# Optimization experiments

Measured on AMD Instinct MI355X. Metric: run time of the kernel, lower is better.

## Reference

```python
import jax, jax.numpy as jnp
import numpy as np

B, N, D, H, DEPTH, MLP_DIM = 8, 1024, 256, 8, 4, 1024
INNER = D * H  # quirk of this repo: inner_dim = dim * n_heads
LN_EPS = 1e-3  # keras LayerNormalization default epsilon


def setup_inputs() -> dict:
    key = jax.random.key(0)
    ks = jax.random.split(key, 6)
    def nrm(k, shape, s=0.02):
        return jax.random.normal(k, shape, dtype=jnp.float32) * s
    return {
        "x": jax.random.normal(ks[0], (B, N, D), dtype=jnp.float32),
        # PreNorm LayerNorm(axis=1): params have shape (N,) per layer
        "ln1_g": jnp.ones((DEPTH, N), jnp.float32),
        "ln1_b": jnp.zeros((DEPTH, N), jnp.float32),
        "w_qkv": nrm(ks[1], (DEPTH, D, 3 * INNER)),
        "w_out": nrm(ks[2], (DEPTH, INNER, D)),
        "b_out": jnp.zeros((DEPTH, D), jnp.float32),
        "ln2_g": jnp.ones((DEPTH, N), jnp.float32),
        "ln2_b": jnp.zeros((DEPTH, N), jnp.float32),
        "w1": nrm(ks[3], (DEPTH, D, MLP_DIM)),
        "b1": jnp.zeros((DEPTH, MLP_DIM), jnp.float32),
        "w2": nrm(ks[4], (DEPTH, MLP_DIM, D)),
        "b2": jnp.zeros((DEPTH, D), jnp.float32),
    }


def _ln_axis1(x, g, b):
    # keras LayerNormalization(axis=1): normalize over sequence axis
    mu = jnp.mean(x, axis=1, keepdims=True)
    var = jnp.var(x, axis=1, keepdims=True)
    return (x - mu) * jax.lax.rsqrt(var + LN_EPS) * g[None, :, None] + b[None, :, None]


def _split_heads(t):
    # b n (h d) -> b h n d, with per-head dim d == D
    return t.reshape(B, N, H, D).transpose(0, 2, 1, 3)


def reference(x, ln1_g, ln1_b, w_qkv, w_out, b_out, ln2_g, ln2_b, w1, b1, w2, b2):
    scale = D ** -0.5
    for i in range(DEPTH):
        # --- PreNorm + MHA ---
        h = _ln_axis1(x, ln1_g[i], ln1_b[i])
        qkv = h @ w_qkv[i]                               # [B,N,3*INNER]
        q, k, v = jnp.split(qkv, 3, axis=-1)
        q, k, v = _split_heads(q), _split_heads(k), _split_heads(v)
        dot = jnp.einsum('bhid,bhjd->bhij', q, k) * scale  # [B,H,N,N]
        A = jax.nn.softmax(dot, axis=-1)
        z = jnp.einsum('bhij,bhjd->bhid', A, v)
        z = z.transpose(0, 2, 1, 3).reshape(B, N, INNER)
        x = x + z @ w_out[i] + b_out[i]
        # --- PreNorm + MLP (exact erf GELU) ---
        h = _ln_axis1(x, ln2_g[i], ln2_b[i])
        h = jax.nn.gelu(h @ w1[i] + b1[i], approximate=False)
        x = x + h @ w2[i] + b2[i]
    return x
```

## Files before the change

kernel.cpp:

```cpp
#include <hip/hip_runtime.h>
#include <hip/hip_bf16.h>

#define SEQ    1024
#define DM     256
#define NH     8
#define NB     8
#define NLAYER 4
#define MLPD   1024
#define ROWS   (NB*SEQ)
#define QKVW   6144
#define INNERW 2048

typedef __attribute__((ext_vector_type(8))) short bh8;
typedef __attribute__((ext_vector_type(4))) short bh4;
typedef __attribute__((ext_vector_type(4))) float fx4;

__device__ __forceinline__ short f2bf(float f) {
  return __builtin_bit_cast(short, __float2bfloat16(f));
}
__device__ __forceinline__ fx4 mfma16(bh8 a, bh8 b, fx4 c) {
  return __builtin_amdgcn_mfma_f32_16x16x32_bf16(a, b, c, 0, 0, 0);
}
__device__ __forceinline__ void g2l16(const void* g, void* l) {
  __builtin_amdgcn_global_load_lds(
      (const __attribute__((address_space(1))) void*)g,
      (__attribute__((address_space(3))) void*)l, 16, 0, 0);
}
__device__ __forceinline__ int kperm(int r) {
  return ((r & 1) << 2) | ((r >> 1) & 3);
}

__global__ void wtrans_k(const float* __restrict__ src, __hip_bfloat16* __restrict__ dst,
                         int R, int C, size_t sls, size_t dls) {
  src += (size_t)blockIdx.z * sls;
  dst += (size_t)blockIdx.z * dls;
  __shared__ float t[32][33];
  int tx = threadIdx.x, ty = threadIdx.y;
  int r0 = blockIdx.y * 32, c0 = blockIdx.x * 32;
#pragma unroll
  for (int i = 0; i < 32; i += 8) t[ty + i][tx] = src[(size_t)(r0 + ty + i) * C + c0 + tx];
  __syncthreads();
#pragma unroll
  for (int i = 0; i < 32; i += 8)
    dst[(size_t)(c0 + ty + i) * R + r0 + tx] = __float2bfloat16(t[tx][ty + i]);
}

__global__ void ln_k(const float* __restrict__ xf, const float* __restrict__ gam,
                     const float* __restrict__ bet, __hip_bfloat16* __restrict__ h) {
  int b = blockIdx.y, d0 = blockIdx.x * 8;
  int dl = threadIdx.x & 1;
  int nt = threadIdx.x >> 1;
  const float* xb = xf + (size_t)b * SEQ * DM + d0 + dl * 4;
  fx4 s = 0.f, ss = 0.f;
  for (int n = nt; n < SEQ; n += 128) {
    fx4 v = *(const fx4*)(xb + (size_t)n * DM);
    s += v; ss += v * v;
  }
  __shared__ fx4 S1[128][2], S2[128][2];
  __shared__ fx4 MU[2], RS[2];
  S1[nt][dl] = s; S2[nt][dl] = ss;
  __syncthreads();
  if (nt < 16) {
    fx4 a = S1[nt][dl], c = S2[nt][dl];
#pragma unroll
    for (int i = 0; i < 7; i++) { a += S1[nt + 16 + i * 16][dl]; c += S2[nt + 16 + i * 16][dl]; }
    S1[nt][dl] = a; S2[nt][dl] = c;
  }
  __syncthreads();
  if (nt == 0) {
    fx4 a = 0.f, c = 0.f;
#pragma unroll
    for (int i = 0; i < 16; i++) { a += S1[i][dl]; c += S2[i][dl]; }
    fx4 mu, rs;
#pragma unroll
    for (int r = 0; r < 4; r++) {
      mu[r] = a[r] * (1.f / SEQ);
      float var = c[r] * (1.f / SEQ) - mu[r] * mu[r];
      rs[r] = rsqrtf(var + 1e-3f);
    }
    MU[dl] = mu; RS[dl] = rs;
  }
  __syncthreads();
  fx4 mu = MU[dl], rs = RS[dl];
  __hip_bfloat16* hb = h + (size_t)b * SEQ * DM + d0 + dl * 4;
  for (int n = nt; n < SEQ; n += 128) {
    fx4 v = *(const fx4*)(xb + (size_t)n * DM);
    float gn = gam[n], bn = bet[n];
    bh4 o;
#pragma unroll
    for (int r = 0; r < 4; r++) o[r] = f2bf((v[r] - mu[r]) * rs[r] * gn + bn);
    *(bh4*)(hb + (size_t)n * DM) = o;
  }
}

template <int BM, int BN, int EPI, int DBUF>
__global__ __launch_bounds__(256) void gemm_bt(
    const __hip_bfloat16* __restrict__ A, const __hip_bfloat16* __restrict__ Bt,
    __hip_bfloat16* __restrict__ Cout, const float* __restrict__ bias,
    const float* __restrict__ rin, float* __restrict__ rout,
    __hip_bfloat16* __restrict__ vT, int M, int Nc, int K) {
  constexpr int BK = 64;
  constexpr int NR = BN / 32;
  constexpr int MR = BM / 32;
  constexpr int SPAN = (BM + BN) * BK;
  static_assert(BN == 64 || BN == 128, "");
  static_assert(BM == 64 || BM == 128, "");
  constexpr int LDSE = (EPI == 3) ? 128 * 132 : SPAN * (DBUF ? 2 : 1);
  __shared__ __hip_bfloat16 smem[LDSE];
  const int tid = threadIdx.x;
  const int lane = tid & 63, w = tid >> 6;
  const int g = lane >> 4, qr = lane & 15;
  const int wr = w >> 1, wc = w & 1;
  const unsigned aid = blockIdx.y * gridDim.x + blockIdx.x;
  const unsigned nwg = gridDim.x * gridDim.y;
  const unsigned lid = (aid & 7u) * (nwg >> 3) + (aid >> 3);
  const int m0 = (int)(lid / gridDim.x) * BM, n0 = (int)(lid % gridDim.x) * BN;
  const int swr = kperm(qr & 7);

  fx4 acc[MR][NR];
#pragma unroll
  for (int m = 0; m < MR; m++)
#pragma unroll
    for (int n = 0; n < NR; n++) acc[m][n] = 0.f;

  constexpr int ACH = (BM * BK) / (8 * 256);
  constexpr int BCH = (BN * BK) / (8 * 256);

  auto stage = [&](int buf, int k0) {
    __hip_bfloat16* As_ = smem + buf * SPAN;
    __hip_bfloat16* Bs_ = As_ + BM * BK;
#pragma unroll
    for (int c = 0; c < ACH; c++) {
      int idx = tid + c * 256;
      int row = idx >> 3, gr2 = idx & 7;
      g2l16(A + (size_t)(m0 + row) * K + k0 + ((gr2 ^ kperm(row & 7)) << 3), (char*)As_ + idx * 16);
    }
#pragma unroll
    for (int c = 0; c < BCH; c++) {
      int idx = tid + c * 256;
      int col = idx >> 3, gr2 = idx & 7;
      g2l16(Bt + (size_t)(n0 + col) * K + k0 + ((gr2 ^ kperm(col & 7)) << 3), (char*)Bs_ + idx * 16);
    }
  };
  auto comp = [&](const __hip_bfloat16* As_, const __hip_bfloat16* Bs_) {
#pragma unroll
    for (int ks = 0; ks < 2; ks++) {
      bh8 af[MR], bf[NR];
#pragma unroll
      for (int m = 0; m < MR; m++)
        af[m] = *(const bh8*)(As_ + (wr * (BM / 2) + m * 16 + qr) * BK + (((ks * 4 + g) ^ swr) << 3));
#pragma unroll
      for (int n = 0; n < NR; n++)
        bf[n] = *(const bh8*)(Bs_ + (wc * (BN / 2) + n * 16 + qr) * BK + (((ks * 4 + g) ^ swr) << 3));
#pragma unroll
      for (int m = 0; m < MR; m++)
#pragma unroll
        for (int n = 0; n < NR; n++) acc[m][n] = mfma16(af[m], bf[n], acc[m][n]);
    }
  };

  if constexpr (DBUF) {
    stage(0, 0);
    __syncthreads();
    const int NT = K / BK;
    for (int t = 0; t < NT; ++t) {
      const int cur = t & 1;
      if (t + 1 < NT) stage(cur ^ 1, (t + 1) * BK);
      comp(smem + cur * SPAN, smem + cur * SPAN + BM * BK);
      __syncthreads();
    }
  } else {
    for (int k0 = 0; k0 < K; k0 += BK) {
      __syncthreads();
      stage(0, k0);
      __syncthreads();
      comp(smem, smem + BM * BK);
    }
  }

  if constexpr (EPI == 2) {
#pragma unroll
    for (int n = 0; n < NR; n++) {
      int gc = n0 + wc * (BN / 2) + n * 16 + qr;
      float bv = bias[gc];
#pragma unroll
      for (int m = 0; m < MR; m++) {
        int grb = m0 + wr * (BM / 2) + m * 16 + g * 4;
#pragma unroll
        for (int r = 0; r < 4; r++)
          rout[(size_t)(grb + r) * Nc + gc] = rin[(size_t)(grb + r) * Nc + gc] + acc[m][n][r] + bv;
      }
    }
  } else if (EPI == 3 && n0 >= 4096) {
    __syncthreads();
    __hip_bfloat16* Cs = smem;
#pragma unroll
    for (int n = 0; n < NR; n++) {
      int dl = wc * (BN / 2) + n * 16 + qr;
#pragma unroll
      for (int m = 0; m < MR; m++) {
        int nlp = wr * (BM / 2) + (m >> 1) * 32 + g * 8 + (m & 1) * 4;
        bh4 v;
#pragma unroll
        for (int r = 0; r < 4; r++) v[r] = f2bf(acc[m][n][r]);
        *(bh4*)(Cs + dl * 132 + nlp) = v;
      }
    }
    __syncthreads();
    const int dl = tid >> 1, half = tid & 1;
    const int bb = m0 >> 10;
    const int hh = (n0 - 4096) >> 8;
    const int d0v = (n0 - 4096) & 255;
    __hip_bfloat16* dst =
        vT + ((size_t)(bb * 8 + hh) * 256 + d0v + dl) * SEQ + (m0 & 1023) + half * 64;
#pragma unroll
    for (int j = 0; j < 8; j++)
      *(bh8*)(dst + j * 8) = *(const bh8*)(Cs + dl * 132 + half * 64 + j * 8);
  } else {
#pragma unroll
    for (int n = 0; n < NR; n++) {
      int gc = n0 + wc * (BN / 2) + n * 16 + qr;
      float bv = (EPI == 1) ? bias[gc] : 0.f;
#pragma unroll
      for (int m = 0; m < MR; m++) {
        int grb = m0 + wr * (BM / 2) + m * 16 + g * 4;
#pragma unroll
        for (int r = 0; r < 4; r++) {
          float v = acc[m][n][r];
          if (EPI == 1) {
            v += bv;
            v = 0.5f * v * (1.f + erff(v * 0.70710678118654752f));
          }
          Cout[(size_t)(grb + r) * Nc + gc] = __float2bfloat16(v);
        }
      }
    }
  }
}

__global__ __launch_bounds__(256) void attn_k(
    const __hip_bfloat16* __restrict__ qkv, const __hip_bfloat16* __restrict__ vT,
    __hip_bfloat16* __restrict__ z) {
  __shared__ __hip_bfloat16 Ks[32 * 256];
  __shared__ __hip_bfloat16 Vs[256 * 32];
  const int tid = threadIdx.x;
  const int lane = tid & 63, w = tid >> 6;
  const int g = lane >> 4, qr = lane & 15;
  const unsigned aid = (blockIdx.z * NH + blockIdx.y) * (SEQ / 64) + blockIdx.x;
  const unsigned lid = (aid & 7u) * 128u + (aid >> 3);
  const int qi = lid & 15, hh = (lid >> 4) & 7, b = lid >> 7;
  const int q0 = qi * 64 + w * 16;
  const size_t qkv_b = (size_t)b * SEQ * QKVW;

  bh8 qf[8];
  {
    const __hip_bfloat16* qrow = qkv + qkv_b + (size_t)(q0 + qr) * QKVW + hh * 256 + g * 8;
#pragma unroll
    for (int kd = 0; kd < 8; kd++) qf[kd] = *(const bh8*)(qrow + kd * 32);
  }

  fx4 o[16];
#pragma unroll
  for (int i = 0; i < 16; i++) o[i] = 0.f;
  float m_run = -INFINITY, l_run = 0.f;
  constexpr float cL = 0.0625f * 1.44269504f;

  const int ksw = kperm(qr & 7);
  const int vsw = ((qr >> 1) & 3);

  for (int j0 = 0; j0 < SEQ; j0 += 32) {
    __syncthreads();
#pragma unroll
    for (int c = 0; c < 4; c++) {
      int idx = tid + c * 256;
      int key = idx >> 5, c16 = idx & 31;
      int dp = (c16 ^ kperm(key & 7)) << 3;
      g2l16(qkv + qkv_b + (size_t)(j0 + key) * QKVW + 2048 + hh * 256 + dp, (char*)Ks + idx * 16);
    }
    const __hip_bfloat16* vb = vT + ((size_t)(b * 8 + hh) * 256) * SEQ + j0;
#pragma unroll
    for (int c = 0; c < 4; c++) {
      int idx = tid + c * 256;
      int d = idx >> 2, gr = idx & 3;
      int np = (gr ^ ((d >> 1) & 3)) << 3;
      g2l16(vb + (size_t)d * SEQ + np, (char*)Vs + idx * 16);
    }
    __syncthreads();

    fx4 s0 = 0.f, s1 = 0.f;
#pragma unroll
    for (int kd = 0; kd < 8; kd++) {
      bh8 k0f = *(const bh8*)(Ks + (size_t)qr * 256 + (((kd * 4 + g) ^ ksw) << 3));
      bh8 k1f = *(const bh8*)(Ks + (size_t)(16 + qr) * 256 + (((kd * 4 + g) ^ ksw) << 3));
      s0 = mfma16(k0f, qf[kd], s0);
      s1 = mfma16(k1f, qf[kd], s1);
    }
    float sv[8];
#pragma unroll
    for (int r = 0; r < 4; r++) { sv[r] = s0[r]; sv[4 + r] = s1[r]; }
    float pmax = sv[0];
#pragma unroll
    for (int i = 1; i < 8; i++) pmax = fmaxf(pmax, sv[i]);
    pmax = fmaxf(pmax, __shfl_xor(pmax, 16));
    pmax = fmaxf(pmax, __shfl_xor(pmax, 32));
    if (!__all(pmax <= m_run + 128.f)) {
      float m_new = fmaxf(m_run, pmax);
      float corr = __builtin_amdgcn_exp2f((m_run - m_new) * cL);
#pragma unroll
      for (int nd = 0; nd < 16; nd++) {
        o[nd][0] *= corr; o[nd][1] *= corr; o[nd][2] *= corr; o[nd][3] *= corr;
      }
      l_run *= corr;
      m_run = m_new;
    }
    float mL = m_run * cL;
    float p[8], ps = 0.f;
#pragma unroll
    for (int i = 0; i < 8; i++) {
      p[i] = __builtin_amdgcn_exp2f(fmaf(sv[i], cL, -mL));
      ps += p[i];
    }
    ps += __shfl_xor(ps, 16);
    ps += __shfl_xor(ps, 32);
    l_run += ps;
    bh8 pa;
#pragma unroll
    for (int i = 0; i < 8; i++) pa[i] = f2bf(p[i]);
#pragma unroll
    for (int nd = 0; nd < 16; nd++) {
      int d = nd * 16 + qr;
      bh8 vf = *(const bh8*)(Vs + (size_t)d * 32 + ((g ^ vsw) << 3));
      o[nd] = mfma16(vf, pa, o[nd]);
    }
  }

  float inv = 1.f / l_run;
  __hip_bfloat16* zb = z + (size_t)b * SEQ * INNERW + hh * 256 + (size_t)(q0 + qr) * INNERW;
#pragma unroll
  for (int nd = 0; nd < 16; nd++) {
    bh4 ov;
#pragma unroll
    for (int r = 0; r < 4; r++) ov[r] = f2bf(o[nd][r] * inv);
    *(bh4*)(zb + nd * 16 + g * 4) = ov;
  }
}

extern "C" void kernel_launch(void* const* d_in, const int* in_sizes, int n_in,
                              void* d_out, int out_size, void* d_ws, size_t ws_size,
                              hipStream_t stream) {
  const float* x_in  = (const float*)d_in[0];
  const float* ln1g  = (const float*)d_in[1];
  const float* ln1b  = (const float*)d_in[2];
  const float* w_qkv = (const float*)d_in[3];
  const float* w_out = (const float*)d_in[4];
  const float* b_out = (const float*)d_in[5];
  const float* ln2g  = (const float*)d_in[6];
  const float* ln2b  = (const float*)d_in[7];
  const float* w1    = (const float*)d_in[8];
  const float* b1    = (const float*)d_in[9];
  const float* w2    = (const float*)d_in[10];
  const float* b2    = (const float*)d_in[11];

  char* ws = (char*)d_ws;
  size_t off = 0;
  auto alloc = [&](size_t bytes) { char* p = ws + off; off += (bytes + 255) & ~(size_t)255; return p; };
  float*          xf    = (float*)         alloc((size_t)ROWS * DM * 4);
  __hip_bfloat16* h     = (__hip_bfloat16*)alloc((size_t)ROWS * DM * 2);
  __hip_bfloat16* qkv   = (__hip_bfloat16*)alloc((size_t)ROWS * QKVW * 2);
  __hip_bfloat16* vT    = (__hip_bfloat16*)alloc((size_t)NB * NH * 256 * SEQ * 2);
  __hip_bfloat16* zbuf  = (__hip_bfloat16*)alloc((size_t)ROWS * INNERW * 2);
  __hip_bfloat16* mh    = zbuf;
  __hip_bfloat16* wqkvT = (__hip_bfloat16*)alloc((size_t)NLAYER * QKVW * DM * 2);
  __hip_bfloat16* woutT = (__hip_bfloat16*)alloc((size_t)NLAYER * DM * INNERW * 2);
  __hip_bfloat16* w1T   = (__hip_bfloat16*)alloc((size_t)NLAYER * MLPD * DM * 2);
  __hip_bfloat16* w2T   = (__hip_bfloat16*)alloc((size_t)NLAYER * DM * MLPD * 2);
  (void)ws_size; (void)in_sizes; (void)n_in; (void)out_size;

  wtrans_k<<<dim3(QKVW / 32, DM / 32, NLAYER), dim3(32, 8), 0, stream>>>(
      w_qkv, wqkvT, DM, QKVW, (size_t)DM * QKVW, (size_t)DM * QKVW);
  wtrans_k<<<dim3(DM / 32, INNERW / 32, NLAYER), dim3(32, 8), 0, stream>>>(
      w_out, woutT, INNERW, DM, (size_t)INNERW * DM, (size_t)INNERW * DM);
  wtrans_k<<<dim3(MLPD / 32, DM / 32, NLAYER), dim3(32, 8), 0, stream>>>(
      w1, w1T, DM, MLPD, (size_t)DM * MLPD, (size_t)DM * MLPD);
  wtrans_k<<<dim3(DM / 32, MLPD / 32, NLAYER), dim3(32, 8), 0, stream>>>(
      w2, w2T, MLPD, DM, (size_t)MLPD * DM, (size_t)MLPD * DM);

  for (int i = 0; i < NLAYER; i++) {
    const float* xcur = (i == 0) ? x_in : xf;
    float* xnext_out = (i == NLAYER - 1) ? (float*)d_out : xf;

    ln_k<<<dim3(DM / 8, NB), 256, 0, stream>>>(xcur, ln1g + i * SEQ, ln1b + i * SEQ, h);
    gemm_bt<128, 128, 3, 0><<<dim3(QKVW / 128, ROWS / 128), 256, 0, stream>>>(
        h, wqkvT + (size_t)i * QKVW * DM, qkv, nullptr, nullptr, nullptr, vT, ROWS, QKVW, DM);
    attn_k<<<dim3(SEQ / 64, NH, NB), 256, 0, stream>>>(qkv, vT, zbuf);
    gemm_bt<64, 64, 2, 1><<<dim3(DM / 64, ROWS / 64), 256, 0, stream>>>(
        zbuf, woutT + (size_t)i * DM * INNERW, nullptr, b_out + i * DM, xcur, xf, nullptr,
        ROWS, DM, INNERW);
    ln_k<<<dim3(DM / 8, NB), 256, 0, stream>>>(xf, ln2g + i * SEQ, ln2b + i * SEQ, h);
    gemm_bt<64, 128, 1, 1><<<dim3(MLPD / 128, ROWS / 64), 256, 0, stream>>>(
        h, w1T + (size_t)i * MLPD * DM, mh, b1 + i * MLPD, nullptr, nullptr, nullptr,
        ROWS, MLPD, DM);
    gemm_bt<64, 64, 2, 1><<<dim3(DM / 64, ROWS / 64), 256, 0, stream>>>(
        mh, w2T + (size_t)i * DM * MLPD, nullptr, b2 + i * DM, xf, xnext_out, nullptr,
        ROWS, DM, MLPD);
  }
}
```

Before: 961.4 us.

## Fuse LayerNorm statistics into residual GEMM epilogues and retile QKV GEMM

Column sums and sums of squares for the sequence-axis LayerNorm are now accumulated in the residual-add GEMM epilogues through shuffles and global atomics. The LN kernel therefore only normalizes and resets the stats buffers, removing one full read pass over the activations per LayerNorm. A separate stats kernel seeds the first layer. The QKV GEMM also moves from 128x128 single-buffered tiles to 64x128 double-buffered tiles, with the V-transpose epilogue generalized to match. The risks are atomic contention, single-pass variance precision, and floating-point ordering that is no longer deterministic.

```diff
diff --git a/kernel.cpp b/kernel.cpp
--- a/kernel.cpp
+++ b/kernel.cpp
@@ -45,19 +45,17 @@
     dst[(size_t)(c0 + ty + i) * R + r0 + tx] = __float2bfloat16(t[tx][ty + i]);
 }
 
-__global__ void ln_k(const float* __restrict__ xf, const float* __restrict__ gam,
-                     const float* __restrict__ bet, __hip_bfloat16* __restrict__ h) {
+__global__ void stats0_k(const float* __restrict__ x, float* __restrict__ statS,
+                         float* __restrict__ statSS) {
   int b = blockIdx.y, d0 = blockIdx.x * 8;
-  int dl = threadIdx.x & 1;
-  int nt = threadIdx.x >> 1;
-  const float* xb = xf + (size_t)b * SEQ * DM + d0 + dl * 4;
+  int dl = threadIdx.x & 1, nt = threadIdx.x >> 1;
+  const float* xb = x + (size_t)b * SEQ * DM + d0 + dl * 4;
   fx4 s = 0.f, ss = 0.f;
   for (int n = nt; n < SEQ; n += 128) {
     fx4 v = *(const fx4*)(xb + (size_t)n * DM);
     s += v; ss += v * v;
   }
   __shared__ fx4 S1[128][2], S2[128][2];
-  __shared__ fx4 MU[2], RS[2];
   S1[nt][dl] = s; S2[nt][dl] = ss;
   __syncthreads();
   if (nt < 16) {
@@ -71,17 +69,32 @@
     fx4 a = 0.f, c = 0.f;
 #pragma unroll
     for (int i = 0; i < 16; i++) { a += S1[i][dl]; c += S2[i][dl]; }
-    fx4 mu, rs;
-#pragma unroll
-    for (int r = 0; r < 4; r++) {
-      mu[r] = a[r] * (1.f / SEQ);
-      float var = c[r] * (1.f / SEQ) - mu[r] * mu[r];
-      rs[r] = rsqrtf(var + 1e-3f);
-    }
-    MU[dl] = mu; RS[dl] = rs;
+    *(fx4*)(statS + b * DM + d0 + dl * 4) = a;
+    *(fx4*)(statSS + b * DM + d0 + dl * 4) = c;
+  }
+}
+
+__global__ void ln_k(const float* __restrict__ xf, const float* __restrict__ gam,
+                     const float* __restrict__ bet, __hip_bfloat16* __restrict__ h,
+                     float* __restrict__ statS, float* __restrict__ statSS) {
+  int b = blockIdx.y, d0 = blockIdx.x * 8;
+  int dl = threadIdx.x & 1;
+  int nt = threadIdx.x >> 1;
+  fx4 s = *(const fx4*)(statS + b * DM + d0 + dl * 4);
+  fx4 ss = *(const fx4*)(statSS + b * DM + d0 + dl * 4);
+  fx4 mu, rs;
+#pragma unroll
+  for (int r = 0; r < 4; r++) {
+    mu[r] = s[r] * (1.f / SEQ);
+    float var = ss[r] * (1.f / SEQ) - mu[r] * mu[r];
+    rs[r] = rsqrtf(var + 1e-3f);
   }
   __syncthreads();
-  fx4 mu = MU[dl], rs = RS[dl];
+  if (threadIdx.x < 2) {
+    *(fx4*)(statS + b * DM + d0 + threadIdx.x * 4) = fx4{0.f, 0.f, 0.f, 0.f};
+    *(fx4*)(statSS + b * DM + d0 + threadIdx.x * 4) = fx4{0.f, 0.f, 0.f, 0.f};
+  }
+  const float* xb = xf + (size_t)b * SEQ * DM + d0 + dl * 4;
   __hip_bfloat16* hb = h + (size_t)b * SEQ * DM + d0 + dl * 4;
   for (int n = nt; n < SEQ; n += 128) {
     fx4 v = *(const fx4*)(xb + (size_t)n * DM);
@@ -98,14 +111,17 @@
     const __hip_bfloat16* __restrict__ A, const __hip_bfloat16* __restrict__ Bt,
     __hip_bfloat16* __restrict__ Cout, const float* __restrict__ bias,
     const float* __restrict__ rin, float* __restrict__ rout,
-    __hip_bfloat16* __restrict__ vT, int M, int Nc, int K) {
+    __hip_bfloat16* __restrict__ vT, float* __restrict__ statS,
+    float* __restrict__ statSS, int M, int Nc, int K) {
   constexpr int BK = 64;
   constexpr int NR = BN / 32;
   constexpr int MR = BM / 32;
   constexpr int SPAN = (BM + BN) * BK;
+  constexpr int CP = BM + 4;
   static_assert(BN == 64 || BN == 128, "");
   static_assert(BM == 64 || BM == 128, "");
-  constexpr int LDSE = (EPI == 3) ? 128 * 132 : SPAN * (DBUF ? 2 : 1);
+  constexpr int BUFE = SPAN * (DBUF ? 2 : 1);
+  constexpr int LDSE = (EPI == 3) ? (BUFE > 128 * CP ? BUFE : 128 * CP) : BUFE;
   __shared__ __hip_bfloat16 smem[LDSE];
   const int tid = threadIdx.x;
   const int lane = tid & 63, w = tid >> 6;
@@ -179,6 +195,9 @@
   }
 
   if constexpr (EPI == 2) {
+    float psum[NR], psq[NR];
+#pragma unroll
+    for (int n = 0; n < NR; n++) { psum[n] = 0.f; psq[n] = 0.f; }
 #pragma unroll
     for (int n = 0; n < NR; n++) {
       int gc = n0 + wc * (BN / 2) + n * 16 + qr;
@@ -187,8 +206,26 @@
       for (int m = 0; m < MR; m++) {
         int grb = m0 + wr * (BM / 2) + m * 16 + g * 4;
 #pragma unroll
-        for (int r = 0; r < 4; r++)
-          rout[(size_t)(grb + r) * Nc + gc] = rin[(size_t)(grb + r) * Nc + gc] + acc[m][n][r] + bv;
+        for (int r = 0; r < 4; r++) {
+          float v = rin[(size_t)(grb + r) * Nc + gc] + acc[m][n][r] + bv;
+          rout[(size_t)(grb + r) * Nc + gc] = v;
+          psum[n] += v; psq[n] += v * v;
+        }
+      }
+    }
+    if (statS) {
+      int b = m0 >> 10;
+#pragma unroll
+      for (int n = 0; n < NR; n++) {
+        int gc = n0 + wc * (BN / 2) + n * 16 + qr;
+        float a = psum[n];
+        a += __shfl_xor(a, 16); a += __shfl_xor(a, 32);
+        float c = psq[n];
+        c += __shfl_xor(c, 16); c += __shfl_xor(c, 32);
+        if (g == 0) {
+          atomicAdd(statS + b * DM + gc, a);
+          atomicAdd(statSS + b * DM + gc, c);
+        }
       }
     }
   } else if (EPI == 3 && n0 >= 4096) {
@@ -199,11 +236,12 @@
       int dl = wc * (BN / 2) + n * 16 + qr;
 #pragma unroll
       for (int m = 0; m < MR; m++) {
-        int nlp = wr * (BM / 2) + (m >> 1) * 32 + g * 8 + (m & 1) * 4;
+        int grp = (wr * (BM / 2) + m * 16) & ~31;
+        int nlp = grp + g * 8 + (m & 1) * 4;
         bh4 v;
 #pragma unroll
         for (int r = 0; r < 4; r++) v[r] = f2bf(acc[m][n][r]);
-        *(bh4*)(Cs + dl * 132 + nlp) = v;
+        *(bh4*)(Cs + dl * CP + nlp) = v;
       }
     }
     __syncthreads();
@@ -212,10 +250,10 @@
     const int hh = (n0 - 4096) >> 8;
     const int d0v = (n0 - 4096) & 255;
     __hip_bfloat16* dst =
-        vT + ((size_t)(bb * 8 + hh) * 256 + d0v + dl) * SEQ + (m0 & 1023) + half * 64;
-#pragma unroll
-    for (int j = 0; j < 8; j++)
-      *(bh8*)(dst + j * 8) = *(const bh8*)(Cs + dl * 132 + half * 64 + j * 8);
+        vT + ((size_t)(bb * 8 + hh) * 256 + d0v + dl) * SEQ + (m0 & 1023) + half * (BM / 2);
+#pragma unroll
+    for (int j = 0; j < BM / 16; j++)
+      *(bh8*)(dst + j * 8) = *(const bh8*)(Cs + dl * CP + half * (BM / 2) + j * 8);
   } else {
 #pragma unroll
     for (int n = 0; n < NR; n++) {
@@ -374,6 +412,8 @@
   __hip_bfloat16* woutT = (__hip_bfloat16*)alloc((size_t)NLAYER * DM * INNERW * 2);
   __hip_bfloat16* w1T   = (__hip_bfloat16*)alloc((size_t)NLAYER * MLPD * DM * 2);
   __hip_bfloat16* w2T   = (__hip_bfloat16*)alloc((size_t)NLAYER * DM * MLPD * 2);
+  float*          statS = (float*)         alloc((size_t)NB * DM * 4);
+  float*          statSS= (float*)         alloc((size_t)NB * DM * 4);
   (void)ws_size; (void)in_sizes; (void)n_in; (void)out_size;
 
   wtrans_k<<<dim3(QKVW / 32, DM / 32, NLAYER), dim3(32, 8), 0, stream>>>(
@@ -385,23 +425,30 @@
   wtrans_k<<<dim3(DM / 32, MLPD / 32, NLAYER), dim3(32, 8), 0, stream>>>(
       w2, w2T, MLPD, DM, (size_t)MLPD * DM, (size_t)MLPD * DM);
 
+  stats0_k<<<dim3(DM / 8, NB), 256, 0, stream>>>(x_in, statS, statSS);
+
   for (int i = 0; i < NLAYER; i++) {
     const float* xcur = (i == 0) ? x_in : xf;
     float* xnext_out = (i == NLAYER - 1) ? (float*)d_out : xf;
-
-    ln_k<<<dim3(DM / 8, NB), 256, 0, stream>>>(xcur, ln1g + i * SEQ, ln1b + i * SEQ, h);
-    gemm_bt<128, 128, 3, 0><<<dim3(QKVW / 128, ROWS / 128), 256, 0, stream>>>(
-        h, wqkvT + (size_t)i * QKVW * DM, qkv, nullptr, nullptr, nullptr, vT, ROWS, QKVW, DM);
+    float* sS = (i == NLAYER - 1) ? nullptr : statS;
+    float* sSS = (i == NLAYER - 1) ? nullptr : statSS;
+
+    ln_k<<<dim3(DM / 8, NB), 256, 0, stream>>>(xcur, ln1g + i * SEQ, ln1b + i * SEQ, h,
+                                               statS, statSS);
+    gemm_bt<64, 128, 3, 1><<<dim3(QKVW / 128, ROWS / 64), 256, 0, stream>>>(
+        h, wqkvT + (size_t)i * QKVW * DM, qkv, nullptr, nullptr, nullptr, vT,
+        nullptr, nullptr, ROWS, QKVW, DM);
     attn_k<<<dim3(SEQ / 64, NH, NB), 256, 0, stream>>>(qkv, vT, zbuf);
     gemm_bt<64, 64, 2, 1><<<dim3(DM / 64, ROWS / 64), 256, 0, stream>>>(
         zbuf, woutT + (size_t)i * DM * INNERW, nullptr, b_out + i * DM, xcur, xf, nullptr,
-        ROWS, DM, INNERW);
-    ln_k<<<dim3(DM / 8, NB), 256, 0, stream>>>(xf, ln2g + i * SEQ, ln2b + i * SEQ, h);
+        statS, statSS, ROWS, DM, INNERW);
+    ln_k<<<dim3(DM / 8, NB), 256, 0, stream>>>(xf, ln2g + i * SEQ, ln2b + i * SEQ, h,
+                                               statS, statSS);
     gemm_bt<64, 128, 1, 1><<<dim3(MLPD / 128, ROWS / 64), 256, 0, stream>>>(
         h, w1T + (size_t)i * MLPD * DM, mh, b1 + i * MLPD, nullptr, nullptr, nullptr,
-        ROWS, MLPD, DM);
+        nullptr, nullptr, ROWS, MLPD, DM);
     gemm_bt<64, 64, 2, 1><<<dim3(DM / 64, ROWS / 64), 256, 0, stream>>>(
         mh, w2T + (size_t)i * DM * MLPD, nullptr, b2 + i * DM, xf, xnext_out, nullptr,
-        ROWS, DM, MLPD);
-  }
-}
+        sS, sSS, ROWS, DM, MLPD);
+  }
+}
```

Result: faster. 942.5 us (-2.0%).
